# Optimization experiments

Hardware: AMD Instinct MI355X
Metric: run time of the kernel (lower is better)

## Reference

```python
import jax, jax.numpy as jnp
import numpy as np

B, H, S, E = 4, 16, 4096, 128


def setup_inputs() -> dict:
    key = jax.random.key(0)
    k1, k2 = jax.random.split(key)
    x = jax.random.normal(k1, (B, H, S, E), dtype=jnp.float32)
    coord_positions = jnp.arange(S, dtype=jnp.float32)
    S_cayley = 0.01 * jax.random.normal(k2, (E, E), dtype=jnp.float32)
    return {"x": x, "coord_positions": coord_positions, "S_cayley": S_cayley}


def reference(x, coord_positions, S_cayley):
    embed_dim = x.shape[-1]
    # Cayley transform: P = (I + A)^{-1} (I - A), A antisymmetric -> P orthogonal
    A = (S_cayley - S_cayley.T) / 2.0
    I = jnp.eye(embed_dim, dtype=x.dtype)
    P = jnp.linalg.solve(I + A, I - A)
    # Learned orthogonal projection applied to every token vector
    xt = jnp.matmul(x, P.T)  # (B, H, S, E)
    # RoPE-style rotation with rotate-half convention
    freqs = 1.0 / 10000 ** (jnp.arange(0, embed_dim // 2, dtype=jnp.float32) * 2 / embed_dim)
    angles = jnp.outer(coord_positions, freqs)          # (S, E/2)
    cos_vals = jnp.repeat(jnp.cos(angles), 2, axis=-1)  # (S, E)
    sin_vals = jnp.repeat(jnp.sin(angles), 2, axis=-1)  # (S, E)
    x1, x2 = jnp.split(xt, 2, axis=-1)
    x_perm = jnp.concatenate([-x2, x1], axis=-1)
    return xt * cos_vals[None, None, :, :] + x_perm * sin_vals[None, None, :, :]
```

## Files before the change

### kernel.cpp

```cpp
#include <hip/hip_runtime.h>
#include <hip/hip_bf16.h>
#include <cstdint>
#include <cstddef>

#define S_LEN 4096
#define E_DIM 128
#define NROWS (4 * 16 * 4096)
#define GRID_MAIN 512
#define ITERS 8

typedef __attribute__((ext_vector_type(8))) short bh8;
typedef __attribute__((ext_vector_type(4))) float f4;
typedef unsigned short u16;

__device__ __forceinline__ u16 f2bf(float f) {
    union { float f; uint32_t u; } v; v.f = f;
    uint32_t r = v.u + 0x7FFFu + ((v.u >> 16) & 1u);
    return (u16)(r >> 16);
}
__device__ __forceinline__ short bfc(float f) {
    __hip_bfloat16 h = __float2bfloat16(f);
    return *reinterpret_cast<short*>(&h);
}
__device__ __forceinline__ float bf2f(u16 u) {
    union { uint32_t u; float f; } v; v.u = ((uint32_t)u) << 16;
    return v.f;
}

__device__ __forceinline__ bh8 ldsRow(const u16* M, int row, int c) {
    return *(const bh8*)(&M[row * 128 + ((c ^ (row & 15)) * 8)]);
}
__device__ __forceinline__ int swzIdx(int n, int m) {
    return n * 128 + (((m >> 3) ^ (n & 15)) * 8) + (m & 7);
}

__global__ __launch_bounds__(1024) void k_pro(const float* __restrict__ Sc,
        const float* __restrict__ pos, u16* __restrict__ Qb,
        float* __restrict__ csT) {
    if (blockIdx.x != 0) {
        int t = (blockIdx.x - 1) * 1024 + threadIdx.x;
        for (int e = t; e < S_LEN * 64; e += 16 * 1024) {
            int s = e >> 6, f = e & 63;
            float freq = exp2f(-0.20762050593046015f * (float)f);
            float sv, cv;
            sincosf(pos[s] * freq, &sv, &cv);
            csT[s * 128 + 2 * f]     = cv;
            csT[s * 128 + 2 * f + 1] = sv;
        }
        return;
    }
    __shared__ u16 Abf[128 * 128];
    __shared__ u16 A2bf[128 * 128];
    __shared__ u16 Y1bf[128 * 128];
    __shared__ u16 A4bf[128 * 128];

    for (int e = threadIdx.x; e < 16384; e += 1024) {
        int i = e >> 7, j = e & 127;
        float a = 0.5f * (Sc[i * 128 + j] - Sc[j * 128 + i]);
        Abf[swzIdx(i, j)] = f2bf(a);
    }
    __syncthreads();

    const int wave = threadIdx.x >> 6;
    const int lane = threadIdx.x & 63;
    const int lhi = lane >> 4, llo = lane & 15;
    const int sm = wave & 7;
    const int nh = wave >> 3;

    {
        f4 acc[4];
        #pragma unroll
        for (int t = 0; t < 4; ++t) { f4 z = {0.f,0.f,0.f,0.f}; acc[t] = z; }
        #pragma unroll
        for (int kk = 0; kk < 4; ++kk) {
            bh8 yf = ldsRow(Abf, sm * 16 + llo, kk * 4 + lhi);
            #pragma unroll
            for (int t = 0; t < 4; ++t) {
                bh8 xf = ldsRow(Abf, (nh * 4 + t) * 16 + llo, kk * 4 + lhi);
                acc[t] = __builtin_amdgcn_mfma_f32_16x16x32_bf16(xf, yf, acc[t], 0, 0, 0);
            }
        }
        __syncthreads();
        #pragma unroll
        for (int t = 0; t < 4; ++t)
            #pragma unroll
            for (int r = 0; r < 4; ++r) {
                int n = (nh * 4 + t) * 16 + lhi * 4 + r, m = sm * 16 + llo;
                float a2 = -acc[t][r];
                A2bf[swzIdx(n, m)] = f2bf(a2);
                Y1bf[swzIdx(n, m)] = f2bf(a2 + bf2f(Abf[swzIdx(n, m)]));
            }
    }
    __syncthreads();
    {
        f4 acc[4];
        #pragma unroll
        for (int t = 0; t < 4; ++t) { f4 z = {0.f,0.f,0.f,0.f}; acc[t] = z; }
        #pragma unroll
        for (int kk = 0; kk < 4; ++kk) {
            bh8 yf = ldsRow(A2bf, sm * 16 + llo, kk * 4 + lhi);
            #pragma unroll
            for (int t = 0; t < 4; ++t) {
                bh8 xf = ldsRow(A2bf, (nh * 4 + t) * 16 + llo, kk * 4 + lhi);
                acc[t] = __builtin_amdgcn_mfma_f32_16x16x32_bf16(xf, yf, acc[t], 0, 0, 0);
            }
        }
        #pragma unroll
        for (int t = 0; t < 4; ++t)
            #pragma unroll
            for (int r = 0; r < 4; ++r) {
                int n = (nh * 4 + t) * 16 + lhi * 4 + r, m = sm * 16 + llo;
                A4bf[swzIdx(n, m)] = f2bf(acc[t][r]);
            }
    }
    __syncthreads();
    {
        f4 acc[4];
        #pragma unroll
        for (int t = 0; t < 4; ++t) { f4 z = {0.f,0.f,0.f,0.f}; acc[t] = z; }
        #pragma unroll
        for (int kk = 0; kk < 4; ++kk) {
            bh8 yf = ldsRow(Y1bf, sm * 16 + llo, kk * 4 + lhi);
            #pragma unroll
            for (int t = 0; t < 4; ++t) {
                bh8 xf = ldsRow(A2bf, (nh * 4 + t) * 16 + llo, kk * 4 + lhi);
                acc[t] = __builtin_amdgcn_mfma_f32_16x16x32_bf16(xf, yf, acc[t], 0, 0, 0);
            }
        }
        #pragma unroll
        for (int kk = 0; kk < 4; ++kk) {
            bh8 yf = ldsRow(Y1bf, sm * 16 + llo, kk * 4 + lhi);
            #pragma unroll
            for (int t = 0; t < 4; ++t) {
                bh8 xf = ldsRow(A4bf, (nh * 4 + t) * 16 + llo, kk * 4 + lhi);
                acc[t] = __builtin_amdgcn_mfma_f32_16x16x32_bf16(xf, yf, acc[t], 0, 0, 0);
            }
        }
        #pragma unroll
        for (int t = 0; t < 4; ++t)
            #pragma unroll
            for (int r = 0; r < 4; ++r) {
                int n = (nh * 4 + t) * 16 + lhi * 4 + r, m = sm * 16 + llo;
                float q = 2.0f * (acc[t][r] + bf2f(A2bf[swzIdx(n, m)])
                                            - bf2f(Abf[swzIdx(n, m)]));
                Qb[n * 128 + m] = f2bf(q);
            }
    }
}

__device__ __forceinline__ void iter_body(int it, f4 (&xs)[8],
        const float* __restrict__ x, const float* __restrict__ csT,
        float* __restrict__ out, const u16* Plds, f4* scr,
        int wbase0, int half, int c, int lhi, int llo, float sg) {
    const int wbase = wbase0 + it * 64;

    f4 cs[8];
    #pragma unroll
    for (int j = 0; j < 8; ++j) {
        int s = (wbase + 2 * j + half) & (S_LEN - 1);
        cs[j] = *(const f4*)(csT + (size_t)s * 128 + 4 * c);
    }
    __builtin_amdgcn_sched_barrier(0);

    #pragma unroll
    for (int j = 0; j < 8; ++j) {
        int tk = 2 * j + half;
        scr[tk * 32 + (c ^ tk)] = xs[j];
    }
    bh8 frag[4];
    #pragma unroll
    for (int kk = 0; kk < 4; ++kk) {
        int ch0 = kk * 8 + lhi * 2;
        f4 v0 = scr[llo * 32 + (ch0 ^ llo)];
        f4 v1 = scr[llo * 32 + ((ch0 + 1) ^ llo)];
        bh8 a;
        #pragma unroll
        for (int e = 0; e < 4; ++e) { a[e] = bfc(v0[e]); a[4 + e] = bfc(v1[e]); }
        frag[kk] = a;
    }
    __builtin_amdgcn_sched_barrier(0);

    f4 acc[8];
    #pragma unroll
    for (int t = 0; t < 8; ++t) { f4 z = {0.f, 0.f, 0.f, 0.f}; acc[t] = z; }
    #pragma unroll
    for (int kk = 0; kk < 4; ++kk) {
        #pragma unroll
        for (int t = 0; t < 8; ++t) {
            int pc = (kk * 4 + lhi) ^ llo;
            bh8 qfrag = *(const bh8*)(&Plds[(t * 16 + llo) * 128 + pc * 8]);
            acc[t] = __builtin_amdgcn_mfma_f32_16x16x32_bf16(qfrag, frag[kk], acc[t], 0, 0, 0);
        }
    }

    #pragma unroll
    for (int t = 0; t < 4; ++t) {
        scr[llo * 32 + ((t * 4 + lhi) ^ llo)]      = acc[t];
        scr[llo * 32 + ((16 + t * 4 + lhi) ^ llo)] = acc[t + 4];
    }
    f4 os[8];
    #pragma unroll
    for (int j = 0; j < 8; ++j) {
        int tk = 2 * j + half;
        os[j] = scr[tk * 32 + (c ^ tk)];
    }

    float* ob = out + (size_t)wbase * E_DIM;
    #pragma unroll
    for (int j = 0; j < 8; ++j) {
        f4 xt, xp, o;
        #pragma unroll
        for (int e = 0; e < 4; ++e) xt[e] = os[j][e] + xs[j][e];
        #pragma unroll
        for (int e = 0; e < 4; ++e) xp[e] = __shfl_xor(xt[e], 16, 64);
        #pragma unroll
        for (int e = 0; e < 4; ++e) {
            float cv = cs[j][2 * (e >> 1)];
            float sv = cs[j][2 * (e >> 1) + 1];
            o[e] = xt[e] * cv + sg * xp[e] * sv;
        }
        __builtin_nontemporal_store(o, (f4*)(ob + (2 * j + half) * E_DIM + 4 * c));
    }
    __builtin_amdgcn_sched_barrier(0);

    if (it + 2 < ITERS) {
        const float* xb = x + (size_t)(wbase + 128) * E_DIM;
        #pragma unroll
        for (int j = 0; j < 8; ++j)
            xs[j] = *(const f4*)(xb + (2 * j + half) * E_DIM + 4 * c);
    }
}

__global__ __launch_bounds__(256, 2) void k_main(const float* __restrict__ x,
        const u16* __restrict__ Qb, const float* __restrict__ csT,
        float* __restrict__ out) {
    __shared__ u16 Plds[128 * 128];
    __shared__ f4 scratch[4][16 * 32];

    #pragma unroll
    for (int i = 0; i < 8; ++i) {
        int chunk = i * 256 + threadIdx.x;
        int row = chunk >> 4, cc = chunk & 15;
        int pc = cc ^ (row & 15);
        bh8 v = *(const bh8*)(Qb + chunk * 8);
        *(bh8*)(&Plds[row * 128 + pc * 8]) = v;
    }

    const int wave = threadIdx.x >> 6;
    const int lane = threadIdx.x & 63;
    const int lhi = (lane >> 4) & 3, llo = lane & 15;
    const int half = lane >> 5;
    const int c = lane & 31;
    f4* scr = scratch[wave];

    const int wbase0 = blockIdx.x * 512 + wave * 16;
    const float sg = (lane & 16) ? 1.0f : -1.0f;

    f4 xsA[8], xsB[8];
    {
        const float* xb = x + (size_t)wbase0 * E_DIM;
        #pragma unroll
        for (int j = 0; j < 8; ++j)
            xsA[j] = *(const f4*)(xb + (2 * j + half) * E_DIM + 4 * c);
        const float* xb1 = x + (size_t)(wbase0 + 64) * E_DIM;
        #pragma unroll
        for (int j = 0; j < 8; ++j)
            xsB[j] = *(const f4*)(xb1 + (2 * j + half) * E_DIM + 4 * c);
    }
    __syncthreads();

    #pragma unroll 1
    for (int it2 = 0; it2 < ITERS; it2 += 2) {
        iter_body(it2,     xsA, x, csT, out, Plds, scr, wbase0, half, c, lhi, llo, sg);
        iter_body(it2 + 1, xsB, x, csT, out, Plds, scr, wbase0, half, c, lhi, llo, sg);
    }
}

extern "C" void kernel_launch(void* const* d_in, const int* in_sizes, int n_in,
                              void* d_out, int out_size, void* d_ws, size_t ws_size,
                              hipStream_t stream) {
    const float* x   = (const float*)d_in[0];
    const float* pos = (const float*)d_in[1];
    const float* Sc  = (const float*)d_in[2];
    float* out = (float*)d_out;

    char* ws = (char*)d_ws;
    u16* Qb     = (u16*)(ws);
    float* csT  = (float*)(ws + 32768);

    k_pro<<<17, 1024, 0, stream>>>(Sc, pos, Qb, csT);
    k_main<<<GRID_MAIN, 256, 0, stream>>>(x, Qb, csT, out);
}
```

Baseline: 61.36 us.

## Apply rotary epilogue in MFMA accumulator layout and fully unroll iterations

The RoPE rotation is now computed directly on the MFMA accumulator fragments. Each lane holds matching low and high half columns (acc[t] and acc[t+4]), so the cross-lane shuffle and sign select go away, and cos/sin are loaded per fragment after the MMA. The fp32 residual x is read back from the LDS scratch that was staged for the bf16 conversion, and the rotated result is written to scratch and then read out for coalesced stores. The iteration loop is fully unrolled through a template parameter. The cost is larger code size and possibly higher register pressure, and the cos/sin loads now sit on the critical path after the MMA instead of being issued early.

After: 62.19 us. Within noise of the previous version (+1.3%).

```diff
diff --git a/kernel.cpp b/kernel.cpp
--- a/kernel.cpp
+++ b/kernel.cpp
@@ -148,19 +148,14 @@
     }
 }
 
-__device__ __forceinline__ void iter_body(int it, f4 (&xs)[8],
+template <int IT>
+__device__ __forceinline__ void iter_body(f4 (&xs)[8],
         const float* __restrict__ x, const float* __restrict__ csT,
         float* __restrict__ out, const u16* Plds, f4* scr,
-        int wbase0, int half, int c, int lhi, int llo, float sg) {
-    const int wbase = wbase0 + it * 64;
-
-    f4 cs[8];
-    #pragma unroll
-    for (int j = 0; j < 8; ++j) {
-        int s = (wbase + 2 * j + half) & (S_LEN - 1);
-        cs[j] = *(const f4*)(csT + (size_t)s * 128 + 4 * c);
-    }
-    __builtin_amdgcn_sched_barrier(0);
+        int wbase0, int half, int c, int lhi, int llo) {
+    const int wbase = wbase0 + IT * 64;
+    const int m = wbase + llo;
+    const int s = m & (S_LEN - 1);
 
     #pragma unroll
     for (int j = 0; j < 8; ++j) {
@@ -192,38 +187,41 @@
             acc[t] = __builtin_amdgcn_mfma_f32_16x16x32_bf16(qfrag, frag[kk], acc[t], 0, 0, 0);
         }
     }
-
+    __builtin_amdgcn_sched_barrier(0);
+
+    const float* csp = csT + (size_t)s * 128;
     #pragma unroll
     for (int t = 0; t < 4; ++t) {
-        scr[llo * 32 + ((t * 4 + lhi) ^ llo)]      = acc[t];
-        scr[llo * 32 + ((16 + t * 4 + lhi) ^ llo)] = acc[t + 4];
-    }
-    f4 os[8];
+        const int n0 = t * 16 + lhi * 4;
+        const int cl = t * 4 + lhi;
+        f4 xlo = scr[llo * 32 + (cl ^ llo)];
+        f4 xhi = scr[llo * 32 + ((16 + cl) ^ llo)];
+        f4 cs_lo = *(const f4*)(csp + n0);
+        f4 cs_hi = *(const f4*)(csp + 64 + n0);
+        f4 olo, ohi;
+        #pragma unroll
+        for (int r = 0; r < 4; ++r) {
+            float xt1 = acc[t][r] + xlo[r];
+            float xt2 = acc[t + 4][r] + xhi[r];
+            float c1 = cs_lo[(r >> 1) * 2], s1 = cs_lo[(r >> 1) * 2 + 1];
+            float c2 = cs_hi[(r >> 1) * 2], s2 = cs_hi[(r >> 1) * 2 + 1];
+            olo[r] = xt1 * c1 - xt2 * s1;
+            ohi[r] = xt2 * c2 + xt1 * s2;
+        }
+        scr[llo * 32 + (cl ^ llo)] = olo;
+        scr[llo * 32 + ((16 + cl) ^ llo)] = ohi;
+    }
+
+    float* ob = out + (size_t)wbase * E_DIM;
     #pragma unroll
     for (int j = 0; j < 8; ++j) {
         int tk = 2 * j + half;
-        os[j] = scr[tk * 32 + (c ^ tk)];
-    }
-
-    float* ob = out + (size_t)wbase * E_DIM;
-    #pragma unroll
-    for (int j = 0; j < 8; ++j) {
-        f4 xt, xp, o;
-        #pragma unroll
-        for (int e = 0; e < 4; ++e) xt[e] = os[j][e] + xs[j][e];
-        #pragma unroll
-        for (int e = 0; e < 4; ++e) xp[e] = __shfl_xor(xt[e], 16, 64);
-        #pragma unroll
-        for (int e = 0; e < 4; ++e) {
-            float cv = cs[j][2 * (e >> 1)];
-            float sv = cs[j][2 * (e >> 1) + 1];
-            o[e] = xt[e] * cv + sg * xp[e] * sv;
-        }
+        f4 o = scr[tk * 32 + (c ^ tk)];
         __builtin_nontemporal_store(o, (f4*)(ob + (2 * j + half) * E_DIM + 4 * c));
     }
     __builtin_amdgcn_sched_barrier(0);
 
-    if (it + 2 < ITERS) {
+    if constexpr (IT + 2 < ITERS) {
         const float* xb = x + (size_t)(wbase + 128) * E_DIM;
         #pragma unroll
         for (int j = 0; j < 8; ++j)
@@ -254,26 +252,28 @@
     f4* scr = scratch[wave];
 
     const int wbase0 = blockIdx.x * 512 + wave * 16;
-    const float sg = (lane & 16) ? 1.0f : -1.0f;
 
     f4 xsA[8], xsB[8];
     {
-        const float* xb = x + (size_t)wbase0 * E_DIM;
+        const float* xb0 = x + (size_t)wbase0 * E_DIM;
+        const float* xb1 = xb0 + 64 * E_DIM;
         #pragma unroll
         for (int j = 0; j < 8; ++j)
-            xsA[j] = *(const f4*)(xb + (2 * j + half) * E_DIM + 4 * c);
-        const float* xb1 = x + (size_t)(wbase0 + 64) * E_DIM;
+            xsA[j] = *(const f4*)(xb0 + (2 * j + half) * E_DIM + 4 * c);
         #pragma unroll
         for (int j = 0; j < 8; ++j)
             xsB[j] = *(const f4*)(xb1 + (2 * j + half) * E_DIM + 4 * c);
     }
     __syncthreads();
 
-    #pragma unroll 1
-    for (int it2 = 0; it2 < ITERS; it2 += 2) {
-        iter_body(it2,     xsA, x, csT, out, Plds, scr, wbase0, half, c, lhi, llo, sg);
-        iter_body(it2 + 1, xsB, x, csT, out, Plds, scr, wbase0, half, c, lhi, llo, sg);
-    }
+    iter_body<0>(xsA, x, csT, out, Plds, scr, wbase0, half, c, lhi, llo);
+    iter_body<1>(xsB, x, csT, out, Plds, scr, wbase0, half, c, lhi, llo);
+    iter_body<2>(xsA, x, csT, out, Plds, scr, wbase0, half, c, lhi, llo);
+    iter_body<3>(xsB, x, csT, out, Plds, scr, wbase0, half, c, lhi, llo);
+    iter_body<4>(xsA, x, csT, out, Plds, scr, wbase0, half, c, lhi, llo);
+    iter_body<5>(xsB, x, csT, out, Plds, scr, wbase0, half, c, lhi, llo);
+    iter_body<6>(xsA, x, csT, out, Plds, scr, wbase0, half, c, lhi, llo);
+    iter_body<7>(xsB, x, csT, out, Plds, scr, wbase0, half, c, lhi, llo);
 }
 
 extern "C" void kernel_launch(void* const* d_in, const int* in_sizes, int n_in,
```
